# Kernel optimization log

Measured on AMD Instinct MI355X. Metric: run time of the kernel, lower is better.

Reference implementation:

```python
import jax, jax.numpy as jnp
import numpy as np
import math

N = 512; D = 256; L = 6; H = 8; BINS = 64; LAM = 30.0; STEPS = 8; VOCAB = 20


def _pe(n, d):
    pos = jnp.arange(n, dtype=jnp.float32)[:, None]
    div = jnp.exp(jnp.arange(0, d, 2, dtype=jnp.float32) * (-math.log(10000.0) / d))
    pe = jnp.zeros((n, d), jnp.float32)
    pe = pe.at[:, 0::2].set(jnp.sin(pos * div))
    pe = pe.at[:, 1::2].set(jnp.cos(pos * div))
    return pe


def _ln(x, g, b, eps=1e-5):
    m = x.mean(-1, keepdims=True)
    v = x.var(-1, keepdims=True)
    return (x - m) / jnp.sqrt(v + eps) * g + b


def _gelu(x):
    return jax.nn.gelu(x, approximate=False)  # torch nn.GELU default (erf)


def setup_inputs() -> dict:
    key = jax.random.key(0)
    ks = jax.random.split(key, 20)
    s = 0.02
    nrm = lambda k, sh: jax.random.normal(k, sh, jnp.float32) * s
    z = lambda sh: jnp.zeros(sh, jnp.float32)
    o = lambda sh: jnp.ones(sh, jnp.float32)
    return {
        "tokens": jax.random.randint(ks[0], (1, N), 0, VOCAB),
        "emb": nrm(ks[1], (VOCAB, D)),
        "Wqkv": nrm(ks[2], (L, 3 * D, D)), "bqkv": z((L, 3 * D)),
        "Wo": nrm(ks[3], (L, D, D)), "bo": z((L, D)),
        "g1": o((L, D)), "be1": z((L, D)),
        "W1": nrm(ks[4], (L, 4 * D, D)), "b1": z((L, 4 * D)),
        "W2": nrm(ks[5], (L, D, 4 * D)), "b2": z((L, D)),
        "g2": o((L, D)), "be2": z((L, D)),
        "A1": nrm(ks[6], (D, D)), "a1b": z((D,)),
        "A2": nrm(ks[7], (1, D)), "a2b": z((1,)),
        "Cf": nrm(ks[8], (D, D)), "cb": z((D,)),
        "F1": nrm(ks[9], (D, 2 * D)), "f1b": z((D,)),
        "F2": nrm(ks[10], (BINS, D)), "f2b": z((BINS,)),
        "T1": nrm(ks[11], (D, D)), "t1b": z((D,)),
        "T2": nrm(ks[12], (2, D)), "t2b": z((2,)),
        "Cp": nrm(ks[13], (3, D)), "cpb": z((3,)),
        "noise": jax.random.normal(ks[14], (1, N, 3), jnp.float32),
    }


def reference(tokens, emb, Wqkv, bqkv, Wo, bo, g1, be1, W1, b1, W2, b2, g2, be2,
              A1, a1b, A2, a2b, Cf, cb, F1, f1b, F2, f2b, T1, t1b, T2, t2b,
              Cp, cpb, noise):
    x = emb[tokens] + _pe(N, D)  # [1,N,D]
    dh = D // H
    for l in range(L):  # post-norm TransformerEncoderLayer, ReLU activation
        qkv = x @ Wqkv[l].T + bqkv[l]  # [1,N,3D]
        q, k, v = jnp.split(qkv, 3, axis=-1)
        q = q.reshape(1, N, H, dh).transpose(0, 2, 1, 3)
        k = k.reshape(1, N, H, dh).transpose(0, 2, 1, 3)
        v = v.reshape(1, N, H, dh).transpose(0, 2, 1, 3)
        att = jax.nn.softmax(jnp.einsum('bhqd,bhkd->bhqk', q, k) / math.sqrt(dh), axis=-1)
        o = jnp.einsum('bhqk,bhkd->bhqd', att, v).transpose(0, 2, 1, 3).reshape(1, N, D)
        x = _ln(x + o @ Wo[l].T + bo[l], g1[l], be1[l])
        f = jax.nn.relu(x @ W1[l].T + b1[l]) @ W2[l].T + b2[l]
        x = _ln(x + f, g2[l], be2[l])
    latent = x
    # AdaptiveAlphaPredictor
    ah = _gelu(latent @ A1.T + a1b) @ A2.T + a2b  # [1,N,1]
    alpha = 1.2 + jax.nn.sigmoid(ah)[..., 0] * (3.5 - 1.2)  # [1,N]
    # CSOCRGAttention: power-law x exp-decay kernel over |i-j|
    idx = jnp.arange(N, dtype=jnp.float32)
    r = jnp.abs(idx[:, None] - idx[None, :]) + 1e-4  # [N,N]
    ap = (alpha[:, :, None] + alpha[:, None, :]) * 0.5  # [1,N,N]
    kern = r[None] ** (-ap) * jnp.exp(-r[None] / LAM)
    kern = kern / (kern.sum(-1, keepdims=True) + 1e-8)
    latent = jnp.einsum('bij,bjd->bid', kern, latent)
    # ContactPriorHead
    hh = latent @ Cf.T + cb
    contact = jax.nn.sigmoid(jnp.einsum('bid,bjd->bij', hh, hh))
    # DistogramHead: cat([xi, xj]) @ F1.T == xi @ F1[:, :D].T + xj @ F1[:, D:].T
    hi = latent @ F1[:, :D].T  # [1,N,D]
    hj = latent @ F1[:, D:].T  # [1,N,D]
    ph = _gelu(hi[:, :, None, :] + hj[:, None, :, :] + f1b)  # [1,N,N,D]
    disto = ph @ F2.T + f2b  # [1,N,N,BINS]
    # TorsionGenerator
    t = _gelu(latent @ T1.T + t1b) @ T2.T + t2b  # [1,N,2]
    phi = jnp.tanh(t[..., 0]) * jnp.pi
    psi = jnp.tanh(t[..., 1]) * jnp.pi
    # DiffusionInitializer: fixed small sequential refinement loop
    target = latent @ Cp.T + cpb  # [1,N,3]
    xc = noise
    for tt in reversed(range(STEPS)):
        a = (tt + 1) / STEPS
        xc = a * xc + (1.0 - a) * target
    return latent, alpha, contact, disto, phi, psi, xc


if __name__ == "__main__":
    outs = reference(**setup_inputs())
    for o in outs:
        print(o.shape, o.dtype)
```

## Files before the change

kernel.cpp:

```cpp
#include <hip/hip_runtime.h>
#include <hip/hip_bf16.h>

#define DEV __device__ __forceinline__

typedef float f32x4 __attribute__((ext_vector_type(4)));
typedef short short8 __attribute__((ext_vector_type(8)));
typedef short short4v __attribute__((ext_vector_type(4)));

#if __has_builtin(__builtin_amdgcn_exp2f)
#define EXP2F __builtin_amdgcn_exp2f
#else
#define EXP2F exp2f
#endif
#if __has_builtin(__builtin_amdgcn_rcpf)
#define RCPF __builtin_amdgcn_rcpf
#else
#define RCPF(x) (1.f / (x))
#endif

DEV short f2bf(float f) {
    union { float f; unsigned u; } c; c.f = f;
    unsigned r = (c.u + 0x7FFFu + ((c.u >> 16) & 1u)) >> 16;
    return (short)r;
}

DEV int cvt_pk_bf16(float lo, float hi) {
    int d;
    asm("v_cvt_pk_bf16_f32 %0, %1, %2" : "=v"(d) : "v"(lo), "v"(hi));
    return d;
}

DEV float gelu_fast(float x) {
    float x2 = x * x;
    float y = x * __builtin_fmaf(0.0356774081f, x2, 0.7978845608f);
    y = fminf(fmaxf(y, -15.f), 15.f);
    float e = EXP2F(y * 2.8853900817779268f);
    float r = RCPF(e + 1.f);
    float t = (e - 1.f) * r;
    return 0.5f * x * (1.f + t);
}

DEV float gelu_sig(float x) {
    float e = EXP2F(x * -2.4555282f);
    return x * RCPF(1.f + e);
}

DEV float wred_sum(float v) {
    #pragma unroll
    for (int off = 1; off < 64; off <<= 1) v += __shfl_xor(v, off);
    return v;
}

struct CvtPack {
    const float* s[9];
    short* d[9];
    int n[9];
};
__global__ __launch_bounds__(256) void k_cvt_embed(CvtPack p,
                                                   const int* __restrict__ tokens,
                                                   const float* __restrict__ emb,
                                                   float* __restrict__ x,
                                                   short* __restrict__ xb) {
    if (blockIdx.x < 512) {
        int n = blockIdx.x, d = threadIdx.x;
        int tok = tokens[n];
        float div = expf((float)((d >> 1) * 2) * -0.035977892079030837f);
        float arg = (float)n * div;
        float pe = (d & 1) ? cosf(arg) : sinf(arg);
        float v = emb[tok * 256 + d] + pe;
        x[n * 256 + d] = v;
        xb[n * 256 + d] = f2bf(v);
        return;
    }
    int bid = blockIdx.x - 512;
    #pragma unroll 1
    for (int seg = 0; seg < 9; ++seg) {
        int n4 = p.n[seg] >> 2;
        const float4* src = (const float4*)p.s[seg];
        short4v* dst = (short4v*)p.d[seg];
        for (int i = bid * 256 + threadIdx.x; i < n4; i += 512 * 256) {
            float4 v = src[i];
            short4v o;
            o[0] = f2bf(v.x); o[1] = f2bf(v.y); o[2] = f2bf(v.z); o[3] = f2bf(v.w);
            dst[i] = o;
        }
    }
}

__global__ __launch_bounds__(64) void k_gemm16(const short* __restrict__ A,
                                               const short* __restrict__ W,
                                               const float* __restrict__ bias,
                                               float* __restrict__ outf,
                                               short* __restrict__ outb,
                                               short* __restrict__ vt,
                                               int M, int K, int ldw, int act) {
    int m0 = blockIdx.x * 16, n0 = blockIdx.y * 16;
    int lane = threadIdx.x;
    int cr = lane & 15, g = lane >> 4;
    const short* a0 = A + (size_t)(n0 + cr) * K + g * 8;
    const short* b0 = W + (size_t)(m0 + cr) * ldw + g * 8;
    f32x4 acc = {0.f, 0.f, 0.f, 0.f};
    #pragma unroll 1
    for (int kc = 0; kc < K; kc += 256) {
        short8 af[8], bf8[8];
        #pragma unroll
        for (int ki = 0; ki < 8; ++ki) af[ki] = *(const short8*)(a0 + kc + ki * 32);
        #pragma unroll
        for (int ki = 0; ki < 8; ++ki) bf8[ki] = *(const short8*)(b0 + kc + ki * 32);
        #pragma unroll
        for (int ki = 0; ki < 8; ++ki)
            acc = __builtin_amdgcn_mfma_f32_16x16x32_bf16(af[ki], bf8[ki], acc, 0, 0, 0);
    }
    float bb = bias ? bias[m0 + cr] : 0.f;
    int m = m0 + cr;
    #pragma unroll
    for (int r = 0; r < 4; ++r) {
        int row = n0 + g * 4 + r;
        float v = acc[r] + bb;
        if (act == 1) v = fmaxf(v, 0.f);
        else if (act == 2) v = gelu_fast(v);
        else if (act == 3) v = 1.f / (1.f + __expf(-v));
        if (outf) outf[(size_t)row * M + m] = v;
        if (outb) outb[(size_t)row * M + m] = f2bf(v);
        if (vt && m >= 512) vt[(size_t)(m - 512) * 512 + row] = f2bf(v);
    }
}

__global__ __launch_bounds__(64) void k_attn3(const short* __restrict__ qkvb,
                                              const short* __restrict__ vt,
                                              short* __restrict__ obuf_bf) {
    __shared__ __align__(16) short Pb[16][40];
    int h = blockIdx.x, qt = blockIdx.y;
    int lane = threadIdx.x;
    int cr = lane & 15, g = lane >> 4;
    int qb = qt * 16;
    short8 qf = *(const short8*)(qkvb + (size_t)(qb + cr) * 768 + h * 32 + g * 8);
    f32x4 s[32];
    #pragma unroll
    for (int jt = 0; jt < 32; ++jt) {
        short8 kf = *(const short8*)(qkvb + (size_t)(jt * 16 + cr) * 768 + 256 + h * 32 + g * 8);
        f32x4 z = {0.f, 0.f, 0.f, 0.f};
        s[jt] = __builtin_amdgcn_mfma_f32_16x16x32_bf16(qf, kf, z, 0, 0, 0);
    }
    const float sc = 0.17677669529663687f;
    float m[4], l[4];
    #pragma unroll
    for (int r = 0; r < 4; ++r) {
        float mm = -1e30f;
        #pragma unroll
        for (int jt = 0; jt < 32; ++jt) mm = fmaxf(mm, s[jt][r]);
        #pragma unroll
        for (int off = 1; off < 16; off <<= 1) mm = fmaxf(mm, __shfl_xor(mm, off));
        m[r] = mm * sc;
    }
    #pragma unroll
    for (int r = 0; r < 4; ++r) {
        float ll = 0.f;
        #pragma unroll
        for (int jt = 0; jt < 32; ++jt) {
            float p = __expf(s[jt][r] * sc - m[r]);
            s[jt][r] = p;
            ll += p;
        }
        #pragma unroll
        for (int off = 1; off < 16; off <<= 1) ll += __shfl_xor(ll, off);
        l[r] = ll;
    }
    const short* vth0 = vt + (size_t)(h * 32 + cr) * 512;
    const short* vth1 = vt + (size_t)(h * 32 + 16 + cr) * 512;
    f32x4 o0 = {0.f,0.f,0.f,0.f}, o1 = o0;
    #pragma unroll
    for (int c = 0; c < 16; ++c) {
        #pragma unroll
        for (int r = 0; r < 4; ++r) {
            Pb[4 * g + r][cr]      = f2bf(s[2 * c][r]);
            Pb[4 * g + r][16 + cr] = f2bf(s[2 * c + 1][r]);
        }
        short8 pa = *(const short8*)&Pb[cr][g * 8];
        short8 v0 = *(const short8*)(vth0 + c * 32 + g * 8);
        short8 v1 = *(const short8*)(vth1 + c * 32 + g * 8);
        o0 = __builtin_amdgcn_mfma_f32_16x16x32_bf16(pa, v0, o0, 0, 0, 0);
        o1 = __builtin_amdgcn_mfma_f32_16x16x32_bf16(pa, v1, o1, 0, 0, 0);
    }
    #pragma unroll
    for (int r = 0; r < 4; ++r) {
        float inv = 1.f / l[r];
        int q = qb + 4 * g + r;
        short* op = obuf_bf + (size_t)q * 256 + h * 32;
        op[cr]      = f2bf(o0[r] * inv);
        op[16 + cr] = f2bf(o1[r] * inv);
    }
}

__global__ __launch_bounds__(64) void k_ln(const float* xr, const float* y,
                                           const float* __restrict__ g,
                                           const float* __restrict__ b,
                                           float* out, short* outb) {
    int n = blockIdx.x, lane = threadIdx.x;
    float4 xv = *(const float4*)(xr + (size_t)n * 256 + lane * 4);
    float4 yv = *(const float4*)(y + (size_t)n * 256 + lane * 4);
    float t0 = xv.x + yv.x, t1 = xv.y + yv.y, t2 = xv.z + yv.z, t3 = xv.w + yv.w;
    float s = t0 + t1 + t2 + t3;
    float sq = t0 * t0 + t1 * t1 + t2 * t2 + t3 * t3;
    s = wred_sum(s);
    sq = wred_sum(sq);
    float mean = s * (1.f / 256.f);
    float var = sq * (1.f / 256.f) - mean * mean;
    float rstd = rsqrtf(var + 1e-5f);
    float4 gv = *(const float4*)(g + lane * 4);
    float4 bv = *(const float4*)(b + lane * 4);
    float r0 = (t0 - mean) * rstd * gv.x + bv.x;
    float r1 = (t1 - mean) * rstd * gv.y + bv.y;
    float r2 = (t2 - mean) * rstd * gv.z + bv.z;
    float r3 = (t3 - mean) * rstd * gv.w + bv.w;
    *(float4*)(out + (size_t)n * 256 + lane * 4) = make_float4(r0, r1, r2, r3);
    short4v ob; ob[0] = f2bf(r0); ob[1] = f2bf(r1); ob[2] = f2bf(r2); ob[3] = f2bf(r3);
    *(short4v*)(outb + (size_t)n * 256 + lane * 4) = ob;
}

__global__ __launch_bounds__(64) void k_alpha(const float* __restrict__ g,
                                              const float* __restrict__ A2,
                                              const float* __restrict__ a2b,
                                              float* __restrict__ alpha) {
    int n = blockIdx.x, lane = threadIdx.x;
    float4 gv = *(const float4*)(g + (size_t)n * 256 + lane * 4);
    float4 av = *(const float4*)(A2 + lane * 4);
    float s = gv.x * av.x + gv.y * av.y + gv.z * av.z + gv.w * av.w;
    s = wred_sum(s);
    if (lane == 0) {
        float ah = s + a2b[0];
        alpha[n] = 1.2f + 2.3f / (1.f + __expf(-ah));
    }
}

__global__ __launch_bounds__(256) void k_kern(const float* __restrict__ latent,
                                              const float* __restrict__ alpha,
                                              float* __restrict__ out,
                                              short* __restrict__ outb) {
    __shared__ float wl[512];
    __shared__ float partial[4];
    int i = blockIdx.x, t = threadIdx.x;
    float ai = alpha[i];
    float w0, w1;
    {
        int j = t;
        float dd = fabsf((float)(i - j)) + 1e-4f;
        float ap = 0.5f * (ai + alpha[j]);
        w0 = exp2f(-ap * __log2f(dd) - dd * 0.048089834696298776f);
        j = t + 256;
        dd = fabsf((float)(i - j)) + 1e-4f;
        ap = 0.5f * (ai + alpha[j]);
        w1 = exp2f(-ap * __log2f(dd) - dd * 0.048089834696298776f);
    }
    wl[t] = w0; wl[t + 256] = w1;
    float s = wred_sum(w0 + w1);
    if ((t & 63) == 0) partial[t >> 6] = s;
    __syncthreads();
    float S = partial[0] + partial[1] + partial[2] + partial[3];
    float inv = 1.f / (S + 1e-8f);
    float acc = 0.f;
    #pragma unroll 4
    for (int j = 0; j < 512; ++j) acc += wl[j] * latent[(size_t)j * 256 + t];
    float v = acc * inv;
    out[(size_t)i * 256 + t] = v;
    outb[(size_t)i * 256 + t] = f2bf(v);
}

__global__ __launch_bounds__(512) void k_disto7(const float* __restrict__ hi,
                                                const float* __restrict__ hj,
                                                const short* __restrict__ F2bf,
                                                const float* __restrict__ f2b,
                                                float* __restrict__ out) {
    __shared__ __align__(16) short hjs[16][264];
    int jt = blockIdx.x, it = blockIdx.y;
    int j0 = jt * 16;
    int t = threadIdx.x;
    {
        int r = t >> 5, c = (t & 31) * 8;
        const float* src = hj + (size_t)(j0 + r) * 256 + c;
        float4 v0 = *(const float4*)(src);
        float4 v1 = *(const float4*)(src + 4);
        union { int i[4]; short8 s; } u;
        u.i[0] = cvt_pk_bf16(v0.x, v0.y);
        u.i[1] = cvt_pk_bf16(v0.z, v0.w);
        u.i[2] = cvt_pk_bf16(v1.x, v1.y);
        u.i[3] = cvt_pk_bf16(v1.z, v1.w);
        *(short8*)&hjs[r][c] = u.s;
    }
    __syncthreads();
    int w = t >> 6, lane = t & 63;
    int cr = lane & 15, g = lane >> 4;
    int i0 = it * 16 + w * 2;
    float bb[4];
    #pragma unroll
    for (int c = 0; c < 4; ++c) bb[c] = f2b[c * 16 + cr];
    f32x4 acc[2][4];
    #pragma unroll
    for (int ii = 0; ii < 2; ++ii)
        #pragma unroll
        for (int c = 0; c < 4; ++c) acc[ii][c] = (f32x4){0.f,0.f,0.f,0.f};
    #pragma unroll 1
    for (int ks = 0; ks < 8; ++ks) {
        int kb = ks * 32 + g * 8;
        short8 B[4];
        #pragma unroll
        for (int c = 0; c < 4; ++c)
            B[c] = *(const short8*)(F2bf + (size_t)(c * 16 + cr) * 256 + kb);
        union { short8 s; int i[4]; } jv;
        jv.s = *(const short8*)&hjs[cr][kb];
        float jf[8];
        #pragma unroll
        for (int q = 0; q < 4; ++q) {
            union { int i; float f; } lo, hi2;
            lo.i = jv.i[q] << 16;
            hi2.i = jv.i[q] & 0xffff0000;
            jf[q * 2] = lo.f;
            jf[q * 2 + 1] = hi2.f;
        }
        #pragma unroll
        for (int ii = 0; ii < 2; ++ii) {
            const float* hr = hi + (size_t)(i0 + ii) * 256 + kb;
            float4 ha = *(const float4*)(hr);
            float4 hb = *(const float4*)(hr + 4);
            float p0 = gelu_sig(ha.x + jf[0]);
            float p1 = gelu_sig(ha.y + jf[1]);
            float p2 = gelu_sig(ha.z + jf[2]);
            float p3 = gelu_sig(ha.w + jf[3]);
            float p4 = gelu_sig(hb.x + jf[4]);
            float p5 = gelu_sig(hb.y + jf[5]);
            float p6 = gelu_sig(hb.z + jf[6]);
            float p7 = gelu_sig(hb.w + jf[7]);
            union { int i[4]; short8 s; } u;
            u.i[0] = cvt_pk_bf16(p0, p1);
            u.i[1] = cvt_pk_bf16(p2, p3);
            u.i[2] = cvt_pk_bf16(p4, p5);
            u.i[3] = cvt_pk_bf16(p6, p7);
            #pragma unroll
            for (int c = 0; c < 4; ++c)
                acc[ii][c] = __builtin_amdgcn_mfma_f32_16x16x32_bf16(u.s, B[c], acc[ii][c], 0, 0, 0);
        }
    }
    #pragma unroll
    for (int ii = 0; ii < 2; ++ii) {
        #pragma unroll
        for (int r = 0; r < 4; ++r) {
            int jl = g * 4 + r;
            float* op = out + ((size_t)(i0 + ii) * 512 + j0 + jl) * 64;
            op[cr]      = acc[ii][0][r] + bb[0];
            op[cr + 16] = acc[ii][1][r] + bb[1];
            op[cr + 32] = acc[ii][2][r] + bb[2];
            op[cr + 48] = acc[ii][3][r] + bb[3];
        }
    }
}

__global__ __launch_bounds__(64) void k_torsion(const float* __restrict__ g,
                                                const float* __restrict__ T2,
                                                const float* __restrict__ t2b,
                                                float* __restrict__ phi,
                                                float* __restrict__ psi) {
    int n = blockIdx.x, lane = threadIdx.x;
    float4 gv = *(const float4*)(g + (size_t)n * 256 + lane * 4);
    float4 w0 = *(const float4*)(T2 + lane * 4);
    float4 w1 = *(const float4*)(T2 + 256 + lane * 4);
    float s0 = gv.x * w0.x + gv.y * w0.y + gv.z * w0.z + gv.w * w0.w;
    float s1 = gv.x * w1.x + gv.y * w1.y + gv.z * w1.z + gv.w * w1.w;
    s0 = wred_sum(s0);
    s1 = wred_sum(s1);
    if (lane == 0) {
        phi[n] = tanhf(s0 + t2b[0]) * 3.14159265358979323846f;
        psi[n] = tanhf(s1 + t2b[1]) * 3.14159265358979323846f;
    }
}

__global__ __launch_bounds__(64) void k_diffusion(const float* __restrict__ latent,
                                                  const float* __restrict__ Cp,
                                                  const float* __restrict__ cpb,
                                                  const float* __restrict__ noise,
                                                  float* __restrict__ xc) {
    int n = blockIdx.x, lane = threadIdx.x;
    float4 lv = *(const float4*)(latent + (size_t)n * 256 + lane * 4);
    const float CN = 40320.0f / 16777216.0f;
    float s[3];
    #pragma unroll
    for (int c = 0; c < 3; ++c) {
        float4 w = *(const float4*)(Cp + c * 256 + lane * 4);
        float v = lv.x * w.x + lv.y * w.y + lv.z * w.z + lv.w * w.w;
        s[c] = wred_sum(v);
    }
    if (lane == 0) {
        #pragma unroll
        for (int c = 0; c < 3; ++c) {
            float tg = s[c] + cpb[c];
            xc[n * 3 + c] = CN * noise[n * 3 + c] + (1.f - CN) * tg;
        }
    }
}

extern "C" void kernel_launch(void* const* d_in, const int* in_sizes, int n_in,
                              void* d_out, int out_size, void* d_ws, size_t ws_size,
                              hipStream_t stream) {
    const int*   tokens = (const int*)d_in[0];
    const float* emb  = (const float*)d_in[1];
    const float* Wqkv = (const float*)d_in[2];
    const float* bqkv = (const float*)d_in[3];
    const float* Wo   = (const float*)d_in[4];
    const float* bo   = (const float*)d_in[5];
    const float* g1   = (const float*)d_in[6];
    const float* be1  = (const float*)d_in[7];
    const float* W1   = (const float*)d_in[8];
    const float* b1   = (const float*)d_in[9];
    const float* W2   = (const float*)d_in[10];
    const float* b2   = (const float*)d_in[11];
    const float* g2   = (const float*)d_in[12];
    const float* be2  = (const float*)d_in[13];
    const float* A1   = (const float*)d_in[14];
    const float* a1b  = (const float*)d_in[15];
    const float* A2   = (const float*)d_in[16];
    const float* a2b  = (const float*)d_in[17];
    const float* Cf   = (const float*)d_in[18];
    const float* cb   = (const float*)d_in[19];
    const float* F1   = (const float*)d_in[20];
    const float* f1b  = (const float*)d_in[21];
    const float* F2   = (const float*)d_in[22];
    const float* f2b  = (const float*)d_in[23];
    const float* T1   = (const float*)d_in[24];
    const float* t1b  = (const float*)d_in[25];
    const float* T2   = (const float*)d_in[26];
    const float* t2b  = (const float*)d_in[27];
    const float* Cp   = (const float*)d_in[28];
    const float* cpb  = (const float*)d_in[29];
    const float* noise= (const float*)d_in[30];

    float* ws   = (float*)d_ws;
    float* x    = ws;
    float* y2   = ws + 131072;
    float* gbuf = ws + 262144;
    float* hi   = ws + 393216;
    float* hj   = ws + 524288;
    short* S    = (short*)(ws + 655360);
    short* x_bf    = S;
    short* obuf_bf = S + 131072;
    short* h1_bf   = S + 262144;
    short* hh_bf   = S + 786432;
    short* lat_bf  = S + 917504;
    short* F2bf    = S + 1048576;
    short* qkv_bf  = S + 1064960;
    short* vt      = S + 1458176;
    short* Wqkv_bf = S + 1589248;
    short* Wo_bf   = S + 2768896;
    short* W1_bf   = S + 3162112;
    short* W2_bf   = S + 4734976;
    short* A1_bf   = S + 6307840;
    short* Cf_bf   = S + 6373376;
    short* F1_bf   = S + 6438912;
    short* T1_bf   = S + 6569984;

    float* out = (float*)d_out;
    float* o_latent  = out;
    float* o_alpha   = out + 131072;
    float* o_contact = out + 131584;
    float* o_disto   = out + 393728;
    float* o_phi     = out + 17170944;
    float* o_psi     = out + 17171456;
    float* o_xc      = out + 17171968;

    CvtPack p;
    p.s[0] = Wqkv; p.d[0] = Wqkv_bf; p.n[0] = 1179648;
    p.s[1] = Wo;   p.d[1] = Wo_bf;   p.n[1] = 393216;
    p.s[2] = W1;   p.d[2] = W1_bf;   p.n[2] = 1572864;
    p.s[3] = W2;   p.d[3] = W2_bf;   p.n[3] = 1572864;
    p.s[4] = A1;   p.d[4] = A1_bf;   p.n[4] = 65536;
    p.s[5] = Cf;   p.d[5] = Cf_bf;   p.n[5] = 65536;
    p.s[6] = F1;   p.d[6] = F1_bf;   p.n[6] = 131072;
    p.s[7] = T1;   p.d[7] = T1_bf;   p.n[7] = 65536;
    p.s[8] = F2;   p.d[8] = F2bf;    p.n[8] = 16384;
    k_cvt_embed<<<1024, 256, 0, stream>>>(p, tokens, emb, x, x_bf);

    for (int l = 0; l < 6; ++l) {
        k_gemm16<<<dim3(48, 32), 64, 0, stream>>>(x_bf, Wqkv_bf + (size_t)l * 196608,
            bqkv + l * 768, nullptr, qkv_bf, vt, 768, 256, 256, 0);
        k_attn3<<<dim3(8, 32), 64, 0, stream>>>(qkv_bf, vt, obuf_bf);
        k_gemm16<<<dim3(16, 32), 64, 0, stream>>>(obuf_bf, Wo_bf + (size_t)l * 65536,
            bo + l * 256, y2, nullptr, nullptr, 256, 256, 256, 0);
        k_ln<<<512, 64, 0, stream>>>(x, y2, g1 + l * 256, be1 + l * 256, x, x_bf);
        k_gemm16<<<dim3(64, 32), 64, 0, stream>>>(x_bf, W1_bf + (size_t)l * 262144,
            b1 + l * 1024, nullptr, h1_bf, nullptr, 1024, 256, 256, 1);
        k_gemm16<<<dim3(16, 32), 64, 0, stream>>>(h1_bf, W2_bf + (size_t)l * 262144,
            b2 + l * 256, y2, nullptr, nullptr, 256, 1024, 1024, 0);
        k_ln<<<512, 64, 0, stream>>>(x, y2, g2 + l * 256, be2 + l * 256, x, x_bf);
    }

    k_gemm16<<<dim3(16, 32), 64, 0, stream>>>(x_bf, A1_bf, a1b, gbuf, nullptr, nullptr,
                                              256, 256, 256, 2);
    k_alpha<<<512, 64, 0, stream>>>(gbuf, A2, a2b, o_alpha);
    k_kern<<<512, 256, 0, stream>>>(x, o_alpha, o_latent, lat_bf);
    k_gemm16<<<dim3(16, 32), 64, 0, stream>>>(lat_bf, Cf_bf, cb, nullptr, hh_bf, nullptr,
                                              256, 256, 256, 0);
    k_gemm16<<<dim3(32, 32), 64, 0, stream>>>(hh_bf, hh_bf, nullptr, o_contact, nullptr,
                                              nullptr, 512, 256, 256, 3);
    k_gemm16<<<dim3(16, 32), 64, 0, stream>>>(lat_bf, F1_bf, f1b, hi, nullptr, nullptr,
                                              256, 256, 512, 0);
    k_gemm16<<<dim3(16, 32), 64, 0, stream>>>(lat_bf, F1_bf + 256, nullptr, hj, nullptr,
                                              nullptr, 256, 256, 512, 0);
    k_disto7<<<dim3(32, 32), 512, 0, stream>>>(hi, hj, F2bf, f2b, o_disto);
    k_gemm16<<<dim3(16, 32), 64, 0, stream>>>(lat_bf, T1_bf, t1b, gbuf, nullptr, nullptr,
                                              256, 256, 256, 2);
    k_torsion<<<512, 64, 0, stream>>>(gbuf, T2, t2b, o_phi, o_psi);
    k_diffusion<<<512, 64, 0, stream>>>(o_latent, Cp, cpb, noise, o_xc);
}
```

Measured before the change: 346.2 us.

## Fuse head GEMMs with reductions, merge F1 GEMMs, and prefetch in disto kernel

Result: no change. 353.1 us (+2.0%).

```diff
diff --git a/kernel.cpp b/kernel.cpp
--- a/kernel.cpp
+++ b/kernel.cpp
@@ -123,6 +123,35 @@
         if (outf) outf[(size_t)row * M + m] = v;
         if (outb) outb[(size_t)row * M + m] = f2bf(v);
         if (vt && m >= 512) vt[(size_t)(m - 512) * 512 + row] = f2bf(v);
+    }
+}
+
+__global__ __launch_bounds__(64) void k_gemm_f1(const short* __restrict__ A,
+                                                const short* __restrict__ F1,
+                                                const float* __restrict__ f1b,
+                                                float* __restrict__ hij) {
+    int m0 = blockIdx.x * 16, n0 = blockIdx.y * 16;
+    int lane = threadIdx.x;
+    int cr = lane & 15, g = lane >> 4;
+    const short* a0 = A + (size_t)(n0 + cr) * 256 + g * 8;
+    const short* b0 = (m0 < 256)
+        ? F1 + (size_t)(m0 + cr) * 512 + g * 8
+        : F1 + (size_t)(m0 - 256 + cr) * 512 + 256 + g * 8;
+    f32x4 acc = {0.f, 0.f, 0.f, 0.f};
+    short8 af[8], bf8[8];
+    #pragma unroll
+    for (int ki = 0; ki < 8; ++ki) af[ki] = *(const short8*)(a0 + ki * 32);
+    #pragma unroll
+    for (int ki = 0; ki < 8; ++ki) bf8[ki] = *(const short8*)(b0 + ki * 32);
+    #pragma unroll
+    for (int ki = 0; ki < 8; ++ki)
+        acc = __builtin_amdgcn_mfma_f32_16x16x32_bf16(af[ki], bf8[ki], acc, 0, 0, 0);
+    float bb = (m0 < 256) ? f1b[m0 + cr] : 0.f;
+    int m = m0 + cr;
+    #pragma unroll
+    for (int r = 0; r < 4; ++r) {
+        int row = n0 + g * 4 + r;
+        hij[(size_t)row * 512 + m] = acc[r] + bb;
     }
 }
 
@@ -218,18 +247,81 @@
     *(short4v*)(outb + (size_t)n * 256 + lane * 4) = ob;
 }
 
-__global__ __launch_bounds__(64) void k_alpha(const float* __restrict__ g,
-                                              const float* __restrict__ A2,
-                                              const float* __restrict__ a2b,
-                                              float* __restrict__ alpha) {
-    int n = blockIdx.x, lane = threadIdx.x;
-    float4 gv = *(const float4*)(g + (size_t)n * 256 + lane * 4);
+__global__ __launch_bounds__(1024) void k_alpha2(const short* __restrict__ x_bf,
+                                                 const short* __restrict__ A1_bf,
+                                                 const float* __restrict__ a1b,
+                                                 const float* __restrict__ A2,
+                                                 const float* __restrict__ a2b,
+                                                 float* __restrict__ alpha) {
+    __shared__ float strip[16][260];
+    int n0 = blockIdx.x * 16;
+    int t = threadIdx.x, w = t >> 6, lane = t & 63;
+    int cr = lane & 15, g = lane >> 4;
+    int m0 = w * 16;
+    const short* a0 = x_bf + (size_t)(n0 + cr) * 256 + g * 8;
+    const short* b0 = A1_bf + (size_t)(m0 + cr) * 256 + g * 8;
+    f32x4 acc = {0.f, 0.f, 0.f, 0.f};
+    short8 af[8], bf8[8];
+    #pragma unroll
+    for (int ki = 0; ki < 8; ++ki) af[ki] = *(const short8*)(a0 + ki * 32);
+    #pragma unroll
+    for (int ki = 0; ki < 8; ++ki) bf8[ki] = *(const short8*)(b0 + ki * 32);
+    #pragma unroll
+    for (int ki = 0; ki < 8; ++ki)
+        acc = __builtin_amdgcn_mfma_f32_16x16x32_bf16(af[ki], bf8[ki], acc, 0, 0, 0);
+    float bb = a1b[m0 + cr];
+    #pragma unroll
+    for (int r = 0; r < 4; ++r)
+        strip[g * 4 + r][m0 + cr] = gelu_fast(acc[r] + bb);
+    __syncthreads();
+    float4 sv = *(const float4*)&strip[w][lane * 4];
     float4 av = *(const float4*)(A2 + lane * 4);
-    float s = gv.x * av.x + gv.y * av.y + gv.z * av.z + gv.w * av.w;
+    float s = sv.x * av.x + sv.y * av.y + sv.z * av.z + sv.w * av.w;
     s = wred_sum(s);
     if (lane == 0) {
         float ah = s + a2b[0];
-        alpha[n] = 1.2f + 2.3f / (1.f + __expf(-ah));
+        alpha[n0 + w] = 1.2f + 2.3f / (1.f + __expf(-ah));
+    }
+}
+
+__global__ __launch_bounds__(1024) void k_tors2(const short* __restrict__ lat_bf,
+                                                const short* __restrict__ T1_bf,
+                                                const float* __restrict__ t1b,
+                                                const float* __restrict__ T2,
+                                                const float* __restrict__ t2b,
+                                                float* __restrict__ phi,
+                                                float* __restrict__ psi) {
+    __shared__ float strip[16][260];
+    int n0 = blockIdx.x * 16;
+    int t = threadIdx.x, w = t >> 6, lane = t & 63;
+    int cr = lane & 15, g = lane >> 4;
+    int m0 = w * 16;
+    const short* a0 = lat_bf + (size_t)(n0 + cr) * 256 + g * 8;
+    const short* b0 = T1_bf + (size_t)(m0 + cr) * 256 + g * 8;
+    f32x4 acc = {0.f, 0.f, 0.f, 0.f};
+    short8 af[8], bf8[8];
+    #pragma unroll
+    for (int ki = 0; ki < 8; ++ki) af[ki] = *(const short8*)(a0 + ki * 32);
+    #pragma unroll
+    for (int ki = 0; ki < 8; ++ki) bf8[ki] = *(const short8*)(b0 + ki * 32);
+    #pragma unroll
+    for (int ki = 0; ki < 8; ++ki)
+        acc = __builtin_amdgcn_mfma_f32_16x16x32_bf16(af[ki], bf8[ki], acc, 0, 0, 0);
+    float bb = t1b[m0 + cr];
+    #pragma unroll
+    for (int r = 0; r < 4; ++r)
+        strip[g * 4 + r][m0 + cr] = gelu_fast(acc[r] + bb);
+    __syncthreads();
+    float4 sv = *(const float4*)&strip[w][lane * 4];
+    float4 w0 = *(const float4*)(T2 + lane * 4);
+    float4 w1 = *(const float4*)(T2 + 256 + lane * 4);
+    float s0 = sv.x * w0.x + sv.y * w0.y + sv.z * w0.z + sv.w * w0.w;
+    float s1 = sv.x * w1.x + sv.y * w1.y + sv.z * w1.z + sv.w * w1.w;
+    s0 = wred_sum(s0);
+    s1 = wred_sum(s1);
+    if (lane == 0) {
+        phi[n0 + w] = tanhf(s0 + t2b[0]) * 3.14159265358979323846f;
+        psi[n0 + w] = tanhf(s1 + t2b[1]) * 3.14159265358979323846f;
     }
 }
 
@@ -266,8 +358,7 @@
     outb[(size_t)i * 256 + t] = f2bf(v);
 }
 
-__global__ __launch_bounds__(512) void k_disto7(const float* __restrict__ hi,
-                                                const float* __restrict__ hj,
+__global__ __launch_bounds__(256) void k_disto8(const float* __restrict__ hij,
                                                 const short* __restrict__ F2bf,
                                                 const float* __restrict__ f2b,
                                                 float* __restrict__ out) {
@@ -276,21 +367,30 @@
     int j0 = jt * 16;
     int t = threadIdx.x;
     {
-        int r = t >> 5, c = (t & 31) * 8;
-        const float* src = hj + (size_t)(j0 + r) * 256 + c;
+        int r = t >> 4, c = (t & 15) * 16;
+        const float* src = hij + (size_t)(j0 + r) * 512 + 256 + c;
         float4 v0 = *(const float4*)(src);
         float4 v1 = *(const float4*)(src + 4);
-        union { int i[4]; short8 s; } u;
-        u.i[0] = cvt_pk_bf16(v0.x, v0.y);
-        u.i[1] = cvt_pk_bf16(v0.z, v0.w);
-        u.i[2] = cvt_pk_bf16(v1.x, v1.y);
-        u.i[3] = cvt_pk_bf16(v1.z, v1.w);
-        *(short8*)&hjs[r][c] = u.s;
+        float4 v2 = *(const float4*)(src + 8);
+        float4 v3 = *(const float4*)(src + 12);
+        union { int i[4]; short8 s; } u0, u1;
+        u0.i[0] = cvt_pk_bf16(v0.x, v0.y);
+        u0.i[1] = cvt_pk_bf16(v0.z, v0.w);
+        u0.i[2] = cvt_pk_bf16(v1.x, v1.y);
+        u0.i[3] = cvt_pk_bf16(v1.z, v1.w);
+        u1.i[0] = cvt_pk_bf16(v2.x, v2.y);
+        u1.i[1] = cvt_pk_bf16(v2.z, v2.w);
+        u1.i[2] = cvt_pk_bf16(v3.x, v3.y);
+        u1.i[3] = cvt_pk_bf16(v3.z, v3.w);
+        *(short8*)&hjs[r][c] = u0.s;
+        *(short8*)&hjs[r][c + 8] = u1.s;
     }
     __syncthreads();
     int w = t >> 6, lane = t & 63;
     int cr = lane & 15, g = lane >> 4;
-    int i0 = it * 16 + w * 2;
+    int i0 = it * 8 + w * 2;
+    const float* hr0 = hij + (size_t)i0 * 512;
+    const float* hr1 = hr0 + 512;
     float bb[4];
     #pragma unroll
     for (int c = 0; c < 4; ++c) bb[c] = f2b[c * 16 + cr];
@@ -299,29 +399,43 @@
     for (int ii = 0; ii < 2; ++ii)
         #pragma unroll
         for (int c = 0; c < 4; ++c) acc[ii][c] = (f32x4){0.f,0.f,0.f,0.f};
+    short8 Bp[4]; short8 jp; float4 hap[2], hbp[2];
+    {
+        int kb = g * 8;
+        #pragma unroll
+        for (int c = 0; c < 4; ++c)
+            Bp[c] = *(const short8*)(F2bf + (size_t)(c * 16 + cr) * 256 + kb);
+        jp = *(const short8*)&hjs[cr][kb];
+        hap[0] = *(const float4*)(hr0 + kb); hbp[0] = *(const float4*)(hr0 + kb + 4);
+        hap[1] = *(const float4*)(hr1 + kb); hbp[1] = *(const float4*)(hr1 + kb + 4);
+    }
     #pragma unroll 1
     for (int ks = 0; ks < 8; ++ks) {
-        int kb = ks * 32 + g * 8;
-        short8 B[4];
-        #pragma unroll
-        for (int c = 0; c < 4; ++c)
-            B[c] = *(const short8*)(F2bf + (size_t)(c * 16 + cr) * 256 + kb);
-        union { short8 s; int i[4]; } jv;
-        jv.s = *(const short8*)&hjs[cr][kb];
+        short8 Bc0 = Bp[0], Bc1 = Bp[1], Bc2 = Bp[2], Bc3 = Bp[3];
+        union { short8 s; int i[4]; } jc; jc.s = jp;
+        float4 a0 = hap[0], b0 = hbp[0], a1 = hap[1], b1 = hbp[1];
+        if (ks < 7) {
+            int kn = (ks + 1) * 32 + g * 8;
+            #pragma unroll
+            for (int c = 0; c < 4; ++c)
+                Bp[c] = *(const short8*)(F2bf + (size_t)(c * 16 + cr) * 256 + kn);
+            jp = *(const short8*)&hjs[cr][kn];
+            hap[0] = *(const float4*)(hr0 + kn); hbp[0] = *(const float4*)(hr0 + kn + 4);
+            hap[1] = *(const float4*)(hr1 + kn); hbp[1] = *(const float4*)(hr1 + kn + 4);
+        }
         float jf[8];
         #pragma unroll
         for (int q = 0; q < 4; ++q) {
             union { int i; float f; } lo, hi2;
-            lo.i = jv.i[q] << 16;
-            hi2.i = jv.i[q] & 0xffff0000;
+            lo.i = jc.i[q] << 16;
+            hi2.i = jc.i[q] & 0xffff0000;
             jf[q * 2] = lo.f;
             jf[q * 2 + 1] = hi2.f;
         }
         #pragma unroll
         for (int ii = 0; ii < 2; ++ii) {
-            const float* hr = hi + (size_t)(i0 + ii) * 256 + kb;
-            float4 ha = *(const float4*)(hr);
-            float4 hb = *(const float4*)(hr + 4);
+            float4 ha = (ii == 0) ? a0 : a1;
+            float4 hb = (ii == 0) ? b0 : b1;
             float p0 = gelu_sig(ha.x + jf[0]);
             float p1 = gelu_sig(ha.y + jf[1]);
             float p2 = gelu_sig(ha.z + jf[2]);
@@ -335,9 +449,10 @@
             u.i[1] = cvt_pk_bf16(p2, p3);
             u.i[2] = cvt_pk_bf16(p4, p5);
             u.i[3] = cvt_pk_bf16(p6, p7);
-            #pragma unroll
-            for (int c = 0; c < 4; ++c)
-                acc[ii][c] = __builtin_amdgcn_mfma_f32_16x16x32_bf16(u.s, B[c], acc[ii][c], 0, 0, 0);
+            acc[ii][0] = __builtin_amdgcn_mfma_f32_16x16x32_bf16(u.s, Bc0, acc[ii][0], 0, 0, 0);
+            acc[ii][1] = __builtin_amdgcn_mfma_f32_16x16x32_bf16(u.s, Bc1, acc[ii][1], 0, 0, 0);
+            acc[ii][2] = __builtin_amdgcn_mfma_f32_16x16x32_bf16(u.s, Bc2, acc[ii][2], 0, 0, 0);
+            acc[ii][3] = __builtin_amdgcn_mfma_f32_16x16x32_bf16(u.s, Bc3, acc[ii][3], 0, 0, 0);
         }
     }
     #pragma unroll
@@ -351,25 +466,6 @@
             op[cr + 32] = acc[ii][2][r] + bb[2];
             op[cr + 48] = acc[ii][3][r] + bb[3];
         }
-    }
-}
-
-__global__ __launch_bounds__(64) void k_torsion(const float* __restrict__ g,
-                                                const float* __restrict__ T2,
-                                                const float* __restrict__ t2b,
-                                                float* __restrict__ phi,
-                                                float* __restrict__ psi) {
-    int n = blockIdx.x, lane = threadIdx.x;
-    float4 gv = *(const float4*)(g + (size_t)n * 256 + lane * 4);
-    float4 w0 = *(const float4*)(T2 + lane * 4);
-    float4 w1 = *(const float4*)(T2 + 256 + lane * 4);
-    float s0 = gv.x * w0.x + gv.y * w0.y + gv.z * w0.z + gv.w * w0.w;
-    float s1 = gv.x * w1.x + gv.y * w1.y + gv.z * w1.z + gv.w * w1.w;
-    s0 = wred_sum(s0);
-    s1 = wred_sum(s1);
-    if (lane == 0) {
-        phi[n] = tanhf(s0 + t2b[0]) * 3.14159265358979323846f;
-        psi[n] = tanhf(s1 + t2b[1]) * 3.14159265358979323846f;
     }
 }
 
@@ -435,10 +531,8 @@
     float* ws   = (float*)d_ws;
     float* x    = ws;
     float* y2   = ws + 131072;
-    float* gbuf = ws + 262144;
-    float* hi   = ws + 393216;
-    float* hj   = ws + 524288;
-    short* S    = (short*)(ws + 655360);
+    float* hij  = ws + 262144;
+    short* S    = (short*)(ws + 524288);
     short* x_bf    = S;
     short* obuf_bf = S + 131072;
     short* h1_bf   = S + 262144;
@@ -491,21 +585,14 @@
         k_ln<<<512, 64, 0, stream>>>(x, y2, g2 + l * 256, be2 + l * 256, x, x_bf);
     }
 
-    k_gemm16<<<dim3(16, 32), 64, 0, stream>>>(x_bf, A1_bf, a1b, gbuf, nullptr, nullptr,
-                                              256, 256, 256, 2);
-    k_alpha<<<512, 64, 0, stream>>>(gbuf, A2, a2b, o_alpha);
+    k_alpha2<<<32, 1024, 0, stream>>>(x_bf, A1_bf, a1b, A2, a2b, o_alpha);
     k_kern<<<512, 256, 0, stream>>>(x, o_alpha, o_latent, lat_bf);
     k_gemm16<<<dim3(16, 32), 64, 0, stream>>>(lat_bf, Cf_bf, cb, nullptr, hh_bf, nullptr,
                                               256, 256, 256, 0);
     k_gemm16<<<dim3(32, 32), 64, 0, stream>>>(hh_bf, hh_bf, nullptr, o_contact, nullptr,
                                               nullptr, 512, 256, 256, 3);
-    k_gemm16<<<dim3(16, 32), 64, 0, stream>>>(lat_bf, F1_bf, f1b, hi, nullptr, nullptr,
-                                              256, 256, 512, 0);
-    k_gemm16<<<dim3(16, 32), 64, 0, stream>>>(lat_bf, F1_bf + 256, nullptr, hj, nullptr,
-                                              nullptr, 256, 256, 512, 0);
-    k_disto7<<<dim3(32, 32), 512, 0, stream>>>(hi, hj, F2bf, f2b, o_disto);
-    k_gemm16<<<dim3(16, 32), 64, 0, stream>>>(lat_bf, T1_bf, t1b, gbuf, nullptr, nullptr,
-                                              256, 256, 256, 2);
-    k_torsion<<<512, 64, 0, stream>>>(gbuf, T2, t2b, o_phi, o_psi);
+    k_gemm_f1<<<dim3(32, 32), 64, 0, stream>>>(lat_bf, F1_bf, f1b, hij);
+    k_disto8<<<dim3(32, 64), 256, 0, stream>>>(hij, F2bf, f2b, o_disto);
+    k_tors2<<<32, 1024, 0, stream>>>(lat_bf, T1_bf, t1b, T2, t2b, o_phi, o_psi);
     k_diffusion<<<512, 64, 0, stream>>>(o_latent, Cp, cpb, noise, o_xc);
 }
```
